# Optimization experiments

Hardware: AMD Instinct MI355X
Metric: run time of the kernel (lower is better)

Reference implementation:

```python
import jax, jax.numpy as jnp
import numpy as np

B, S, E, FF, Q = 8, 2048, 768, 3072, 8  # batch, seq, embed_dim, ffn_dim, n_qubits


def setup_inputs() -> dict:
    key = jax.random.key(0)
    k_x, k_phi, k_w1, k_w2 = jax.random.split(key, 4)
    x = jax.random.normal(k_x, (B, S, E), dtype=jnp.float32)
    # trainable RY angles (one per qubit), like tq.RY(has_params=True)
    phi = jax.random.normal(k_phi, (Q,), dtype=jnp.float32)
    # linear1: n_qubits -> ffn_dim ; linear2: ffn_dim -> embed_dim (torch layout [out, in])
    w1 = jax.random.normal(k_w1, (FF, Q), dtype=jnp.float32) / np.sqrt(Q).astype(np.float32)
    b1 = jnp.zeros((FF,), dtype=jnp.float32)
    w2 = jax.random.normal(k_w2, (E, FF), dtype=jnp.float32) / np.sqrt(FF).astype(np.float32)
    b2 = jnp.zeros((E,), dtype=jnp.float32)
    return {"x": x, "phi": phi, "w1": w1, "b1": b1, "w2": w2, "b2": b2}


def reference(x, phi, w1, b1, w2, b2):
    # Quantum block (exact closed form): for each token, encoder applies
    # RY(x_i) on wire i, then a trainable RY(phi_i) on wire i. Starting from
    # |0>^Q this is a product state; RY compose additively and
    # <Z> after RY(theta)|0> == cos(theta). MeasureAll(PauliZ) therefore gives:
    n_qubits = phi.shape[0]
    meas = jnp.cos(x[..., :n_qubits] + phi)          # [B, S, Q]
    # dropout is identity in eval mode
    h = jax.nn.relu(jnp.einsum('bsq,fq->bsf', meas, w1) + b1)  # [B, S, FF]
    return jnp.einsum('bsf,ef->bse', h, w2) + b2               # [B, S, E]
```

## Files before the change

### kernel.cpp

```cpp
#include <hip/hip_runtime.h>
#include <hip/hip_bf16.h>
#include <stdint.h>

#define M_TOK 16384
#define E_DIM 768
#define FF_DIM 3072
#define Q_N 8

typedef __attribute__((ext_vector_type(8))) short bf16x8;
typedef __attribute__((ext_vector_type(4))) float f32x4;

__device__ inline unsigned short f2bf(float f) {
  union { float f; unsigned u; } v; v.f = f;
  unsigned r = v.u + 0x7fffu + ((v.u >> 16) & 1u);
  return (unsigned short)(r >> 16);
}

__global__ __launch_bounds__(256) void cvt_w2(const float* __restrict__ w2,
                                              __hip_bfloat16* __restrict__ w2b) {
  int i = (blockIdx.x * 256 + threadIdx.x) * 4;
  const int n = E_DIM * FF_DIM;
  if (i < n) {
    float4 v = *(const float4*)(w2 + i);
    ushort4 o;
    o.x = f2bf(v.x); o.y = f2bf(v.y); o.z = f2bf(v.z); o.w = f2bf(v.w);
    *(ushort4*)((unsigned short*)w2b + i) = o;
  }
}

__global__ __launch_bounds__(256) void compute_h(const float* __restrict__ x,
                                                 const float* __restrict__ phi,
                                                 const float* __restrict__ w1,
                                                 const float* __restrict__ b1,
                                                 __hip_bfloat16* __restrict__ hout) {
  __shared__ float s_meas[32][8];
  const int t = threadIdx.x;
  const int bm = blockIdx.x / 6;
  const int bf = blockIdx.x % 6;
  const int m0 = bm * 32;
  const int f0 = bf * 512;

  if (t < 64) {
    int m = t >> 1, hh = t & 1;
    float4 v = *(const float4*)(x + (size_t)(m0 + m) * E_DIM + hh * 4);
    float4 p = *(const float4*)(phi + hh * 4);
    s_meas[m][hh * 4 + 0] = __cosf(v.x + p.x);
    s_meas[m][hh * 4 + 1] = __cosf(v.y + p.y);
    s_meas[m][hh * 4 + 2] = __cosf(v.z + p.z);
    s_meas[m][hh * 4 + 3] = __cosf(v.w + p.w);
  }
  __syncthreads();

  const float4* wr = (const float4*)(w1 + (size_t)(f0 + 2 * t) * Q_N);
  float4 a0 = wr[0], a1 = wr[1], b0 = wr[2], b1v = wr[3];
  float wA[8] = {a0.x, a0.y, a0.z, a0.w, a1.x, a1.y, a1.z, a1.w};
  float wB[8] = {b0.x, b0.y, b0.z, b0.w, b1v.x, b1v.y, b1v.z, b1v.w};
  const float biasA = b1[f0 + 2 * t];
  const float biasB = b1[f0 + 2 * t + 1];

  uint32_t* dst32 = (uint32_t*)hout;
  for (int m = 0; m < 32; ++m) {
    float a = biasA, b = biasB;
#pragma unroll
    for (int q = 0; q < 8; ++q) {
      float mv = s_meas[m][q];
      a = fmaf(mv, wA[q], a);
      b = fmaf(mv, wB[q], b);
    }
    a = fmaxf(a, 0.f);
    b = fmaxf(b, 0.f);
    uint32_t pack = (uint32_t)f2bf(a) | ((uint32_t)f2bf(b) << 16);
    dst32[(size_t)(m0 + m) * (FF_DIM / 2) + (f0 / 2) + t] = pack;
  }
}

#define GLDS16(g, l)                                                          \
  __builtin_amdgcn_global_load_lds(                                           \
      (const __attribute__((address_space(1))) void*)(g),                     \
      (__attribute__((address_space(3))) void*)(l), 16, 0, 0)

#define BUF_ELEMS 28672
#define B_OFF 16384

__global__ __launch_bounds__(512, 1) void gemm_bt(const __hip_bfloat16* __restrict__ A,
                                                  const __hip_bfloat16* __restrict__ Bw,
                                                  const float* __restrict__ b2,
                                                  float* __restrict__ C) {
  const int K = FF_DIM;
  const int N = E_DIM;

  __shared__ __align__(16) __hip_bfloat16 lds[2 * BUF_ELEMS];

  const int t = threadIdx.x;
  const int swz = (blockIdx.x & 7) * 32 + (blockIdx.x >> 3);
  const int bm = swz >> 2;
  const int bn = swz & 3;
  const size_t m0 = (size_t)bm * 256;
  const int n0 = bn * 192;

  const int w = t >> 6, l = t & 63;
  const int wr = w >> 1;
  const int wc = w & 1;
  const int lr = l & 15;
  const int lk = l >> 4;

  const int x0 = lk ^ (lr & 7);
  const int x1 = x0 ^ 4;
  const int baseA = (wr * 64 + lr) * 64;
  const int baseB = B_OFF + (wc * 96 + lr) * 64;
  const int offA0 = baseA + x0 * 8, offA1 = baseA + x1 * 8;
  const int offB0 = baseB + x0 * 8, offB1 = baseB + x1 * 8;

  const int rs = t >> 3;
  const int lc = (t & 7) ^ (rs & 7);
  const __hip_bfloat16* sA[4];
  const __hip_bfloat16* sB[3];
#pragma unroll
  for (int s = 0; s < 4; ++s) sA[s] = A + (m0 + s * 64 + rs) * (size_t)K + lc * 8;
#pragma unroll
  for (int s = 0; s < 3; ++s) sB[s] = Bw + ((size_t)n0 + s * 64 + rs) * K + lc * 8;

  f32x4 acc[4][6] = {};

#define STAGE(K0S, WBUF)                                                      \
  {                                                                           \
    __hip_bfloat16* ld = lds + (WBUF) * BUF_ELEMS + t * 8;                    \
    GLDS16(sA[0] + (K0S), ld);                                                \
    GLDS16(sA[1] + (K0S), ld + 4096);                                         \
    GLDS16(sA[2] + (K0S), ld + 8192);                                         \
    GLDS16(sA[3] + (K0S), ld + 12288);                                        \
    GLDS16(sB[0] + (K0S), ld + 16384);                                        \
    GLDS16(sB[1] + (K0S), ld + 20480);                                        \
    GLDS16(sB[2] + (K0S), ld + 24576);                                        \
  }

#define TILE(KT, RBUF, DO_STAGE)                                              \
  {                                                                           \
    if (DO_STAGE) STAGE(((KT) + 1) * 64, (RBUF) ^ 1);                         \
    const __hip_bfloat16* la = lds + (RBUF) * BUF_ELEMS;                      \
    {                                                 \
      bf16x8 fa[4], fb[6];                                                    \
      _Pragma("unroll") for (int mi = 0; mi < 4; ++mi)                        \
          fa[mi] = *(const bf16x8*)(la + offA0 + mi * 1024);                  \
      _Pragma("unroll") for (int ni = 0; ni < 6; ++ni)                        \
          fb[ni] = *(const bf16x8*)(la + offB0 + ni * 1024);                  \
      __builtin_amdgcn_s_setprio(1);                                          \
      _Pragma("unroll") for (int mi = 0; mi < 4; ++mi)                        \
          _Pragma("unroll") for (int ni = 0; ni < 6; ++ni)                    \
              acc[mi][ni] = __builtin_amdgcn_mfma_f32_16x16x32_bf16(          \
                  fa[mi], fb[ni], acc[mi][ni], 0, 0, 0);                      \
      __builtin_amdgcn_s_setprio(0);                                          \
    }                                                                         \
    {                                                 \
      bf16x8 fa[4], fb[6];                                                    \
      _Pragma("unroll") for (int mi = 0; mi < 4; ++mi)                        \
          fa[mi] = *(const bf16x8*)(la + offA1 + mi * 1024);                  \
      _Pragma("unroll") for (int ni = 0; ni < 6; ++ni)                        \
          fb[ni] = *(const bf16x8*)(la + offB1 + ni * 1024);                  \
      __builtin_amdgcn_s_setprio(1);                                          \
      _Pragma("unroll") for (int mi = 0; mi < 4; ++mi)                        \
          _Pragma("unroll") for (int ni = 0; ni < 6; ++ni)                    \
              acc[mi][ni] = __builtin_amdgcn_mfma_f32_16x16x32_bf16(          \
                  fa[mi], fb[ni], acc[mi][ni], 0, 0, 0);                      \
      __builtin_amdgcn_s_setprio(0);                                          \
    }                                                                         \
    asm volatile("s_waitcnt vmcnt(0)" ::: "memory");                          \
    __builtin_amdgcn_s_barrier();                                             \
  }

  STAGE(0, 0);
  asm volatile("s_waitcnt vmcnt(0)" ::: "memory");
  __builtin_amdgcn_s_barrier();

#pragma unroll 1
  for (int tt = 0; tt < 46; tt += 2) {
    TILE(tt + 0, 0, 1);
    TILE(tt + 1, 1, 1);
  }
  TILE(46, 0, 1);
  TILE(47, 1, 0);

#undef TILE
#undef STAGE

#pragma unroll
  for (int mi = 0; mi < 4; ++mi) {
    const size_t row = m0 + wr * 64 + mi * 16 + lk * 4;
#pragma unroll
    for (int ni = 0; ni < 6; ++ni) {
      const int col = n0 + wc * 96 + ni * 16 + lr;
      const float bias = b2[col];
#pragma unroll
      for (int rr = 0; rr < 4; ++rr) {
        C[(row + rr) * N + col] = acc[mi][ni][rr] + bias;
      }
    }
  }
}

__global__ __launch_bounds__(256) void fallback_fused(const float* __restrict__ x,
                                                      const float* __restrict__ phi,
                                                      const float* __restrict__ w1,
                                                      const float* __restrict__ b1,
                                                      const float* __restrict__ w2,
                                                      const float* __restrict__ b2,
                                                      float* __restrict__ out) {
  __shared__ float s_h[FF_DIM];
  __shared__ float s_meas[Q_N];
  const int t = threadIdx.x;
  const size_t m = blockIdx.x;
  if (t < Q_N) s_meas[t] = __cosf(x[m * E_DIM + t] + phi[t]);
  __syncthreads();
  for (int f = t; f < FF_DIM; f += 256) {
    const float4* wr = (const float4*)(w1 + (size_t)f * Q_N);
    float4 a = wr[0], b = wr[1];
    float acc = b1[f];
    acc = fmaf(s_meas[0], a.x, acc); acc = fmaf(s_meas[1], a.y, acc);
    acc = fmaf(s_meas[2], a.z, acc); acc = fmaf(s_meas[3], a.w, acc);
    acc = fmaf(s_meas[4], b.x, acc); acc = fmaf(s_meas[5], b.y, acc);
    acc = fmaf(s_meas[6], b.z, acc); acc = fmaf(s_meas[7], b.w, acc);
    s_h[f] = fmaxf(acc, 0.f);
  }
  __syncthreads();
  for (int e = t; e < E_DIM; e += 256) {
    const float* w2r = w2 + (size_t)e * FF_DIM;
    float acc = b2[e];
    for (int f = 0; f < FF_DIM; f += 4) {
      float4 wv = *(const float4*)(w2r + f);
      acc = fmaf(s_h[f + 0], wv.x, acc);
      acc = fmaf(s_h[f + 1], wv.y, acc);
      acc = fmaf(s_h[f + 2], wv.z, acc);
      acc = fmaf(s_h[f + 3], wv.w, acc);
    }
    out[m * E_DIM + e] = acc;
  }
}

extern "C" void kernel_launch(void* const* d_in, const int* in_sizes, int n_in,
                              void* d_out, int out_size, void* d_ws, size_t ws_size,
                              hipStream_t stream) {
  const float* x   = (const float*)d_in[0];
  const float* phi = (const float*)d_in[1];
  const float* w1  = (const float*)d_in[2];
  const float* b1  = (const float*)d_in[3];
  const float* w2  = (const float*)d_in[4];
  const float* b2  = (const float*)d_in[5];
  float* out = (float*)d_out;

  const size_t H_BYTES   = (size_t)M_TOK * FF_DIM * 2;
  const size_t W2B_BYTES = (size_t)E_DIM * FF_DIM * 2;
  const size_t NEED = H_BYTES + W2B_BYTES;

  if (ws_size >= NEED) {
    __hip_bfloat16* h   = (__hip_bfloat16*)d_ws;
    __hip_bfloat16* w2b = (__hip_bfloat16*)((char*)d_ws + H_BYTES);
    cvt_w2<<<(E_DIM * FF_DIM) / (256 * 4), 256, 0, stream>>>(w2, w2b);
    compute_h<<<(M_TOK / 32) * (FF_DIM / 512), 256, 0, stream>>>(x, phi, w1, b1, h);
    gemm_bt<<<(M_TOK / 256) * (E_DIM / 192), 512, 0, stream>>>(h, w2b, b2, out);
  } else {
    fallback_fused<<<M_TOK, 256, 0, stream>>>(x, phi, w1, b1, w2, b2, out);
  }
}
```

Before: 98.42 us.

## Fuse w2 conversion and hidden computation into one prep kernel with wider stores

Merges the w2 bf16 conversion kernel and the hidden-layer compute kernel into a single launch, with separate block ranges for each task. The hidden computation is reorganized so each block covers 32 full token rows, and each thread writes 8 packed bf16 values as 16-byte stores instead of 4-byte stores. The conversion path now handles 16 elements per thread. This removes one kernel launch and widens global stores, at the cost of each thread reloading w1 and b1 from global memory or cache for every 8-column group.

```diff
diff --git a/kernel.cpp b/kernel.cpp
--- a/kernel.cpp
+++ b/kernel.cpp
@@ -16,29 +16,38 @@
   return (unsigned short)(r >> 16);
 }
 
-__global__ __launch_bounds__(256) void cvt_w2(const float* __restrict__ w2,
-                                              __hip_bfloat16* __restrict__ w2b) {
-  int i = (blockIdx.x * 256 + threadIdx.x) * 4;
-  const int n = E_DIM * FF_DIM;
-  if (i < n) {
-    float4 v = *(const float4*)(w2 + i);
-    ushort4 o;
-    o.x = f2bf(v.x); o.y = f2bf(v.y); o.z = f2bf(v.z); o.w = f2bf(v.w);
-    *(ushort4*)((unsigned short*)w2b + i) = o;
-  }
-}
-
-__global__ __launch_bounds__(256) void compute_h(const float* __restrict__ x,
-                                                 const float* __restrict__ phi,
-                                                 const float* __restrict__ w1,
-                                                 const float* __restrict__ b1,
-                                                 __hip_bfloat16* __restrict__ hout) {
+#define H_BLOCKS 512
+#define CVT_BLOCKS 576
+
+__global__ __launch_bounds__(256) void prep_fused(const float* __restrict__ x,
+                                                  const float* __restrict__ phi,
+                                                  const float* __restrict__ w1,
+                                                  const float* __restrict__ b1,
+                                                  const float* __restrict__ w2,
+                                                  __hip_bfloat16* __restrict__ hout,
+                                                  __hip_bfloat16* __restrict__ w2b) {
+  if (blockIdx.x >= H_BLOCKS) {
+    const int i0 = ((blockIdx.x - H_BLOCKS) * 256 + threadIdx.x) * 16;
+    const float4* src = (const float4*)(w2 + i0);
+    float4 v0 = src[0], v1 = src[1], v2 = src[2], v3 = src[3];
+    uint4 o0, o1;
+    o0.x = (uint32_t)f2bf(v0.x) | ((uint32_t)f2bf(v0.y) << 16);
+    o0.y = (uint32_t)f2bf(v0.z) | ((uint32_t)f2bf(v0.w) << 16);
+    o0.z = (uint32_t)f2bf(v1.x) | ((uint32_t)f2bf(v1.y) << 16);
+    o0.w = (uint32_t)f2bf(v1.z) | ((uint32_t)f2bf(v1.w) << 16);
+    o1.x = (uint32_t)f2bf(v2.x) | ((uint32_t)f2bf(v2.y) << 16);
+    o1.y = (uint32_t)f2bf(v2.z) | ((uint32_t)f2bf(v2.w) << 16);
+    o1.z = (uint32_t)f2bf(v3.x) | ((uint32_t)f2bf(v3.y) << 16);
+    o1.w = (uint32_t)f2bf(v3.z) | ((uint32_t)f2bf(v3.w) << 16);
+    uint4* dst = (uint4*)((unsigned short*)w2b + i0);
+    dst[0] = o0;
+    dst[1] = o1;
+    return;
+  }
+
   __shared__ float s_meas[32][8];
   const int t = threadIdx.x;
-  const int bm = blockIdx.x / 6;
-  const int bf = blockIdx.x % 6;
-  const int m0 = bm * 32;
-  const int f0 = bf * 512;
+  const int m0 = blockIdx.x * 32;
 
   if (t < 64) {
     int m = t >> 1, hh = t & 1;
@@ -51,26 +60,54 @@
   }
   __syncthreads();
 
-  const float4* wr = (const float4*)(w1 + (size_t)(f0 + 2 * t) * Q_N);
-  float4 a0 = wr[0], a1 = wr[1], b0 = wr[2], b1v = wr[3];
-  float wA[8] = {a0.x, a0.y, a0.z, a0.w, a1.x, a1.y, a1.z, a1.w};
-  float wB[8] = {b0.x, b0.y, b0.z, b0.w, b1v.x, b1v.y, b1v.z, b1v.w};
-  const float biasA = b1[f0 + 2 * t];
-  const float biasB = b1[f0 + 2 * t + 1];
-
-  uint32_t* dst32 = (uint32_t*)hout;
-  for (int m = 0; m < 32; ++m) {
-    float a = biasA, b = biasB;
-#pragma unroll
-    for (int q = 0; q < 8; ++q) {
-      float mv = s_meas[m][q];
-      a = fmaf(mv, wA[q], a);
-      b = fmaf(mv, wB[q], b);
+  const int mi = t >> 3;
+  const int fc = t & 7;
+
+  float mv[8];
+  {
+    f32x4 a = *(const f32x4*)&s_meas[mi][0];
+    f32x4 b = *(const f32x4*)&s_meas[mi][4];
+    mv[0] = a[0]; mv[1] = a[1]; mv[2] = a[2]; mv[3] = a[3];
+    mv[4] = b[0]; mv[5] = b[1]; mv[6] = b[2]; mv[7] = b[3];
+  }
+
+  uint4* dst = (uint4*)((unsigned short*)hout + (size_t)(m0 + mi) * FF_DIM);
+#pragma unroll 2
+  for (int fg = fc; fg < FF_DIM / 8; fg += 8) {
+    const float4* wr = (const float4*)(w1 + (size_t)fg * 8 * Q_N);
+    const float4 b1lo = *(const float4*)(b1 + fg * 8);
+    const float4 b1hi = *(const float4*)(b1 + fg * 8 + 4);
+    uint32_t pk[4];
+#pragma unroll
+    for (int j = 0; j < 8; ++j) {
+      float4 a0 = wr[j * 2];
+      float4 a1 = wr[j * 2 + 1];
+      float a;
+      switch (j) {
+        case 0: a = b1lo.x; break;
+        case 1: a = b1lo.y; break;
+        case 2: a = b1lo.z; break;
+        case 3: a = b1lo.w; break;
+        case 4: a = b1hi.x; break;
+        case 5: a = b1hi.y; break;
+        case 6: a = b1hi.z; break;
+        default: a = b1hi.w; break;
+      }
+      a = fmaf(mv[0], a0.x, a);
+      a = fmaf(mv[1], a0.y, a);
+      a = fmaf(mv[2], a0.z, a);
+      a = fmaf(mv[3], a0.w, a);
+      a = fmaf(mv[4], a1.x, a);
+      a = fmaf(mv[5], a1.y, a);
+      a = fmaf(mv[6], a1.z, a);
+      a = fmaf(mv[7], a1.w, a);
+      a = fmaxf(a, 0.f);
+      unsigned short u = f2bf(a);
+      if (j & 1) pk[j >> 1] |= ((uint32_t)u) << 16;
+      else pk[j >> 1] = (uint32_t)u;
     }
-    a = fmaxf(a, 0.f);
-    b = fmaxf(b, 0.f);
-    uint32_t pack = (uint32_t)f2bf(a) | ((uint32_t)f2bf(b) << 16);
-    dst32[(size_t)(m0 + m) * (FF_DIM / 2) + (f0 / 2) + t] = pack;
+    uint4 pv; pv.x = pk[0]; pv.y = pk[1]; pv.z = pk[2]; pv.w = pk[3];
+    dst[fg] = pv;
   }
 }
 
@@ -254,8 +291,8 @@
   if (ws_size >= NEED) {
     __hip_bfloat16* h   = (__hip_bfloat16*)d_ws;
     __hip_bfloat16* w2b = (__hip_bfloat16*)((char*)d_ws + H_BYTES);
-    cvt_w2<<<(E_DIM * FF_DIM) / (256 * 4), 256, 0, stream>>>(w2, w2b);
-    compute_h<<<(M_TOK / 32) * (FF_DIM / 512), 256, 0, stream>>>(x, phi, w1, b1, h);
+    prep_fused<<<H_BLOCKS + CVT_BLOCKS, 256, 0, stream>>>(x, phi, w1, b1, w2,
+                                                          h, w2b);
     gemm_bt<<<(M_TOK / 256) * (E_DIM / 192), 512, 0, stream>>>(h, w2b, b2, out);
   } else {
     fallback_fused<<<M_TOK, 256, 0, stream>>>(x, phi, w1, b1, w2, b2, out);
```

Result: slower. 247.2 us (+151.1%).
